# Kernel optimization log

Measured on AMD Instinct MI355X. Metric: run time of the kernel, lower is better.

## Reference

```python
import jax, jax.numpy as jnp
import numpy as np

C = 256
NUM_HEADS = 8
GROUPS = 32
EPS = 1e-5


def setup_inputs() -> dict:
    key = jax.random.key(0)
    ks = jax.random.split(key, 7)
    B, D, H, W = 1, 16, 16, 16
    x = jax.random.normal(ks[0], (B, C, D, H, W), dtype=jnp.float32)
    # GroupNorm affine params (torch default: weight=1, bias=0; randomize slightly)
    gn_gamma = 1.0 + 0.02 * jax.random.normal(ks[1], (C,), dtype=jnp.float32)
    gn_beta = 0.02 * jax.random.normal(ks[2], (C,), dtype=jnp.float32)
    # 1x1x1 Conv3d == pointwise linear over channels
    qkv_w = jax.random.normal(ks[3], (3 * C, C), dtype=jnp.float32) / np.sqrt(C)
    qkv_b = 0.01 * jax.random.normal(ks[4], (3 * C,), dtype=jnp.float32)
    proj_w = jax.random.normal(ks[5], (C, C), dtype=jnp.float32) / np.sqrt(C)
    proj_b = 0.01 * jax.random.normal(ks[6], (C,), dtype=jnp.float32)
    return {"x": x, "gn_gamma": gn_gamma, "gn_beta": gn_beta,
            "qkv_w": qkv_w, "qkv_b": qkv_b, "proj_w": proj_w, "proj_b": proj_b}


def _group_norm(x, gamma, beta):
    B, Cc, D, H, W = x.shape
    xg = x.reshape(B, GROUPS, -1)  # [B, G, (C/G)*D*H*W]
    mean = xg.mean(axis=2, keepdims=True)
    var = xg.var(axis=2, keepdims=True)
    xn = ((xg - mean) * jax.lax.rsqrt(var + EPS)).reshape(B, Cc, D, H, W)
    return xn * gamma[None, :, None, None, None] + beta[None, :, None, None, None]


def reference(x, gn_gamma, gn_beta, qkv_w, qkv_b, proj_w, proj_b):
    B, Cc, D, H, W = x.shape
    N = D * H * W
    heads = NUM_HEADS
    hd = Cc // heads
    scale = hd ** -0.5

    xn = _group_norm(x, gn_gamma, gn_beta)
    # 1x1x1 conv -> pointwise linear over channel dim
    h = jnp.einsum('bcn,oc->bon', xn.reshape(B, Cc, N), qkv_w) + qkv_b[None, :, None]
    # match torch: reshape(B,3,heads,hd,N).permute(1,0,2,4,3)
    qkv = h.reshape(B, 3, heads, hd, N).transpose(1, 0, 2, 4, 3)  # [3,B,heads,N,hd]
    q, k, v = qkv[0], qkv[1], qkv[2]
    attn = jax.nn.softmax(jnp.einsum('bhnd,bhmd->bhnm', q, k) * scale, axis=-1)
    out = jnp.einsum('bhnm,bhmd->bhnd', attn, v)  # [B,heads,N,hd]
    # match torch: transpose(1,2).reshape(B,C,D,H,W)
    out = out.transpose(0, 2, 1, 3).reshape(B, Cc, D, H, W)
    out = jnp.einsum('bcn,oc->bon', out.reshape(B, Cc, N), proj_w) + proj_b[None, :, None]
    return x + out.reshape(B, Cc, D, H, W)
```

## Files before the change

### kernel.cpp

```cpp
#include <hip/hip_runtime.h>
#include <hip/hip_bf16.h>
#include <cstddef>
#include <cstdint>

#define NTOK 4096
#define CCH  256
#define HEADS 8
#define HD    32
#define QSCALE 0.25503494f

typedef __attribute__((ext_vector_type(8)))  short short8;
typedef __attribute__((ext_vector_type(4)))  short short4v;
typedef __attribute__((ext_vector_type(16))) float f32x16;

__device__ __forceinline__ unsigned short f2bf(float x) {
    unsigned u = __builtin_bit_cast(unsigned, x);
    u = (u + 0x7fffu + ((u >> 16) & 1u)) >> 16;
    return (unsigned short)u;
}
__device__ __forceinline__ unsigned packbf2(float a, float b) {
    unsigned r;
    asm("v_cvt_pk_bf16_f32 %0, %1, %2" : "=v"(r) : "v"(a), "v"(b));
    return r;
}
__device__ __forceinline__ float exp2hw(float x) {
    float r;
    asm("v_exp_f32 %0, %1" : "=v"(r) : "v"(x));
    return r;
}

#define CROW(r, hi) (((r) & 3) + 8 * ((r) >> 2) + 4 * (hi))

__global__ __launch_bounds__(256) void gn_part_kernel(
    const float* __restrict__ X, float2* __restrict__ part)
{
    int c = blockIdx.x, tid = threadIdx.x;
    const float4* xr = (const float4*)(X + (size_t)c * NTOK);
    float s = 0.f, ss = 0.f;
    #pragma unroll
    for (int i = 0; i < 4; i++) {
        float4 v = xr[tid + i * 256];
        s  += (v.x + v.y) + (v.z + v.w);
        ss += (v.x*v.x + v.y*v.y) + (v.z*v.z + v.w*v.w);
    }
    #pragma unroll
    for (int off = 32; off >= 1; off >>= 1) {
        s  += __shfl_down(s, off, 64);
        ss += __shfl_down(ss, off, 64);
    }
    __shared__ float rs[4], rss[4];
    int wid = tid >> 6, lane = tid & 63;
    if (lane == 0) { rs[wid] = s; rss[wid] = ss; }
    __syncthreads();
    if (tid == 0) {
        part[c] = make_float2(rs[0] + rs[1] + rs[2] + rs[3],
                              rss[0] + rss[1] + rss[2] + rss[3]);
    }
}

__global__ __launch_bounds__(256) void prep_kernel(
    const float* __restrict__ X, const float2* __restrict__ part,
    const float* __restrict__ gamma, const float* __restrict__ beta,
    const float* __restrict__ qkvw, const float* __restrict__ projw,
    unsigned short* __restrict__ Xt, unsigned short* __restrict__ Wqb,
    unsigned short* __restrict__ Wpb)
{
    int bi = blockIdx.x, tid = threadIdx.x;
    if (bi >= 256) {
        const float* src; unsigned short* dst;
        if (bi < 268) { src = qkvw + (size_t)(bi - 256) * 16384; dst = Wqb + (size_t)(bi - 256) * 16384; }
        else          { src = projw + (size_t)(bi - 268) * 16384; dst = Wpb + (size_t)(bi - 268) * 16384; }
        #pragma unroll
        for (int i = 0; i < 16; i++) {
            float4 v = *(const float4*)(src + (size_t)tid * 4 + (size_t)i * 1024);
            short4v w;
            w[0] = (short)f2bf(v.x); w[1] = (short)f2bf(v.y);
            w[2] = (short)f2bf(v.z); w[3] = (short)f2bf(v.w);
            *(short4v*)(dst + (size_t)tid * 4 + (size_t)i * 1024) = w;
        }
        return;
    }
    __shared__ float plds[64 * 65];
    __shared__ float gmean[8], grstd[8];
    int ci = bi >> 6, ni = bi & 63;
    if (tid < 8) {
        int g = ci * 8 + tid;
        float s = 0.f, ss = 0.f;
        #pragma unroll
        for (int k = 0; k < 8; k++) {
            float2 p = part[g * 8 + k];
            s += p.x; ss += p.y;
        }
        float mean = s * (1.f / 32768.f);
        float var  = ss * (1.f / 32768.f) - mean * mean;
        gmean[tid] = mean;
        grstd[tid] = rsqrtf(var + 1e-5f);
    }
    __syncthreads();
    #pragma unroll
    for (int i = 0; i < 4; i++) {
        int cl = (tid >> 4) + i * 16;
        int c  = ci * 64 + cl;
        int gl = cl >> 3;
        float scv = gamma[c] * grstd[gl];
        float tcv = beta[c] - gmean[gl] * scv;
        float4 v = *(const float4*)(X + (size_t)c * NTOK + ni * 64 + (tid & 15) * 4);
        float* row = plds + cl * 65 + (tid & 15) * 4;
        row[0] = v.x * scv + tcv; row[1] = v.y * scv + tcv;
        row[2] = v.z * scv + tcv; row[3] = v.w * scv + tcv;
    }
    __syncthreads();
    int nw = tid >> 2, c4 = (tid & 3) * 16;
    unsigned short tmp[16];
    #pragma unroll
    for (int i = 0; i < 16; i++) tmp[i] = f2bf(plds[(c4 + i) * 65 + nw]);
    unsigned short* dst = Xt + (size_t)(ni * 64 + nw) * CCH + ci * 64 + c4;
    *(short8*)dst       = *(short8*)&tmp[0];
    *(short8*)(dst + 8) = *(short8*)&tmp[8];
}

__global__ __launch_bounds__(256) void qkv_mfma_kernel(
    const unsigned short* __restrict__ Wqb, const unsigned short* __restrict__ Xt,
    const float* __restrict__ qkvb,
    unsigned short* __restrict__ Qb, unsigned short* __restrict__ Kbf,
    unsigned short* __restrict__ Vtb)
{
    __shared__ __align__(16) char vlds[16384];
    const int tid = threadIdx.x;
    const int wid = tid >> 6, lane = tid & 63;
    const int l31 = lane & 31, hi = lane >> 5;
    const int bo = blockIdx.x >> 5, ng = blockIdx.x & 31;
    const int o0 = bo * 32;
    const int n0 = ng * 128 + wid * 32;

    const unsigned short* ap = Xt + (size_t)(n0 + l31) * CCH + hi * 8;
    const unsigned short* bp = Wqb + (size_t)(o0 + l31) * CCH + hi * 8;

    f32x16 acc;
    #pragma unroll
    for (int i = 0; i < 16; i++) acc[i] = 0.f;
    #pragma unroll 4
    for (int ks = 0; ks < 16; ks++) {
        short8 af = *(const short8*)(ap + ks * 16);
        short8 bf = *(const short8*)(bp + ks * 16);
        acc = __builtin_amdgcn_mfma_f32_32x32x16_bf16(af, bf, acc, 0, 0, 0);
    }

    const int t3 = bo >> 3;
    const int h  = (o0 >> 5) & 7;
    const float bias = qkvb[o0 + l31];

    if (t3 != 2) {
        unsigned short* dst = ((t3 == 0) ? Qb : Kbf) + (size_t)h * NTOK * HD + l31;
        const float scl = (t3 == 0) ? QSCALE : 1.0f;
        #pragma unroll
        for (int r = 0; r < 16; r++) {
            int n = n0 + CROW(r, hi);
            dst[(size_t)n * HD] = f2bf((acc[r] + bias) * scl);
        }
    } else {
        char* my = vlds + wid * 4096;
        #pragma unroll
        for (int r = 0; r < 16; r++) {
            int row = CROW(r, hi);
            *(float*)(my + row * 128 + ((l31 * 4) ^ ((row & 7) << 4))) = acc[r] + bias;
        }
        unsigned short tmp[16];
        #pragma unroll
        for (int i = 0; i < 16; i++) {
            int n = hi * 16 + i;
            tmp[i] = f2bf(*(const float*)(my + n * 128 + ((l31 * 4) ^ ((n & 7) << 4))));
        }
        unsigned short* vd = Vtb + ((size_t)h * HD + l31) * NTOK + n0 + hi * 16;
        *(short8*)vd       = *(short8*)&tmp[0];
        *(short8*)(vd + 8) = *(short8*)&tmp[8];
    }
}

__global__ __launch_bounds__(256) void attn_mfma_kernel(
    const unsigned short* __restrict__ Qb, const unsigned short* __restrict__ Kbf,
    const unsigned short* __restrict__ Vtb, unsigned short* __restrict__ att_t)
{
    __shared__ float stash[4][64][37];
    __shared__ float lsum[4][64];
    const int tid = threadIdx.x;
    const int wid = tid >> 6, lane = tid & 63;
    const int l31 = lane & 31, hi = lane >> 5;
    const int bid = blockIdx.x;
    const int h    = bid & 7;
    const int g    = bid >> 3;
    const int base = g & 15;
    const int j0   = (g >> 4) * 64;

    const unsigned short* kp = Kbf + ((size_t)h * NTOK + wid * 1024 + l31) * HD + hi * 8;
    const unsigned short* vp = Vtb + ((size_t)h * HD + l31) * NTOK + wid * 1024 + hi * 8;

    const unsigned short* qpA = Qb + ((size_t)h * NTOK + base + 16 * (size_t)(j0 + l31)) * HD + hi * 8;
    const unsigned short* qpB = qpA + (size_t)32 * 16 * HD;
    short8 qfA0 = *(const short8*)qpA;
    short8 qfA1 = *(const short8*)(qpA + 16);
    short8 qfB0 = *(const short8*)qpB;
    short8 qfB1 = *(const short8*)(qpB + 16);

    f32x16 oaccA, oaccB;
    #pragma unroll
    for (int i = 0; i < 16; i++) { oaccA[i] = 0.f; oaccB[i] = 0.f; }
    const f32x16 zero = oaccA;
    float lA = 0.f, lB = 0.f;

#define ATTN_BODY(KF0, KF1, VF0, VF1) do {                                     \
    f32x16 sA = __builtin_amdgcn_mfma_f32_32x32x16_bf16(KF0, qfA0, zero, 0, 0, 0); \
    sA = __builtin_amdgcn_mfma_f32_32x32x16_bf16(KF1, qfA1, sA, 0, 0, 0);      \
    f32x16 sB = __builtin_amdgcn_mfma_f32_32x32x16_bf16(KF0, qfB0, zero, 0, 0, 0); \
    sB = __builtin_amdgcn_mfma_f32_32x32x16_bf16(KF1, qfB1, sB, 0, 0, 0);      \
    float pA[16], pB[16];                                                      \
    _Pragma("unroll") for (int r = 0; r < 16; r++) pA[r] = exp2hw(sA[r]);      \
    _Pragma("unroll") for (int r = 0; r < 16; r++) pB[r] = exp2hw(sB[r]);      \
    lA += (((pA[0]+pA[1]) + (pA[2]+pA[3])) + ((pA[4]+pA[5]) + (pA[6]+pA[7])))  \
        + (((pA[8]+pA[9]) + (pA[10]+pA[11])) + ((pA[12]+pA[13]) + (pA[14]+pA[15]))); \
    lB += (((pB[0]+pB[1]) + (pB[2]+pB[3])) + ((pB[4]+pB[5]) + (pB[6]+pB[7])))  \
        + (((pB[8]+pB[9]) + (pB[10]+pB[11])) + ((pB[12]+pB[13]) + (pB[14]+pB[15]))); \
    _Pragma("unroll")                                                          \
    for (int m = 0; m < 2; m++) {                                              \
        const int b8 = m * 8;                                                  \
        unsigned A0 = packbf2(pA[b8 + 0], pA[b8 + 1]);                         \
        unsigned A1 = packbf2(pA[b8 + 2], pA[b8 + 3]);                         \
        unsigned B0 = packbf2(pA[b8 + 4], pA[b8 + 5]);                         \
        unsigned B1 = packbf2(pA[b8 + 6], pA[b8 + 7]);                         \
        asm volatile("v_permlane32_swap_b32 %0, %1" : "+v"(A0), "+v"(B0));     \
        asm volatile("v_permlane32_swap_b32 %0, %1" : "+v"(A1), "+v"(B1));     \
        union { unsigned u[4]; short8 v; } pa;                                 \
        pa.u[0] = A0; pa.u[1] = A1; pa.u[2] = B0; pa.u[3] = B1;                \
        oaccA = __builtin_amdgcn_mfma_f32_32x32x16_bf16(                       \
            pa.v, (m == 0) ? (VF0) : (VF1), oaccA, 0, 0, 0);                   \
    }                                                                          \
    _Pragma("unroll")                                                          \
    for (int m = 0; m < 2; m++) {                                              \
        const int b8 = m * 8;                                                  \
        unsigned A0 = packbf2(pB[b8 + 0], pB[b8 + 1]);                         \
        unsigned A1 = packbf2(pB[b8 + 2], pB[b8 + 3]);                         \
        unsigned B0 = packbf2(pB[b8 + 4], pB[b8 + 5]);                         \
        unsigned B1 = packbf2(pB[b8 + 6], pB[b8 + 7]);                         \
        asm volatile("v_permlane32_swap_b32 %0, %1" : "+v"(A0), "+v"(B0));     \
        asm volatile("v_permlane32_swap_b32 %0, %1" : "+v"(A1), "+v"(B1));     \
        union { unsigned u[4]; short8 v; } pa;                                 \
        pa.u[0] = A0; pa.u[1] = A1; pa.u[2] = B0; pa.u[3] = B1;                \
        oaccB = __builtin_amdgcn_mfma_f32_32x32x16_bf16(                       \
            pa.v, (m == 0) ? (VF0) : (VF1), oaccB, 0, 0, 0);                   \
    }                                                                          \
} while (0)

    short8 kf0a = *(const short8*)(kp);
    short8 kf1a = *(const short8*)(kp + 16);
    short8 vf0a = *(const short8*)(vp);
    short8 vf1a = *(const short8*)(vp + 16);

    #pragma unroll 1
    for (int t = 0; t < 32; t += 2) {
        const int t1 = t + 1;
        short8 kf0b = *(const short8*)(kp + t1 * 1024);
        short8 kf1b = *(const short8*)(kp + t1 * 1024 + 16);
        short8 vf0b = *(const short8*)(vp + t1 * 32);
        short8 vf1b = *(const short8*)(vp + t1 * 32 + 16);
        ATTN_BODY(kf0a, kf1a, vf0a, vf1a);
        const int t2 = (t + 2 < 32) ? (t + 2) : 31;
        kf0a = *(const short8*)(kp + t2 * 1024);
        kf1a = *(const short8*)(kp + t2 * 1024 + 16);
        vf0a = *(const short8*)(vp + t2 * 32);
        vf1a = *(const short8*)(vp + t2 * 32 + 16);
        ATTN_BODY(kf0b, kf1b, vf0b, vf1b);
    }
#undef ATTN_BODY

    lA += __shfl_xor(lA, 32, 64);
    lB += __shfl_xor(lB, 32, 64);
    #pragma unroll
    for (int r = 0; r < 16; r++) {
        int rowA = CROW(r, hi);
        stash[wid][rowA][l31] = oaccA[r];
        stash[wid][rowA + 32][l31] = oaccB[r];
    }
    if (lane < 32) { lsum[wid][l31] = lA; lsum[wid][32 + l31] = lB; }
    __syncthreads();

    const int d = tid >> 3, q8 = (tid & 7) * 8;
    unsigned short ob[8];
    #pragma unroll
    for (int i = 0; i < 8; i++) {
        int q = q8 + i;
        float lt = (lsum[0][q] + lsum[1][q]) + (lsum[2][q] + lsum[3][q]);
        float a = (stash[0][q][d] + stash[1][q][d]) + (stash[2][q][d] + stash[3][q][d]);
        ob[i] = f2bf(a / lt);
    }
    unsigned short* dst = att_t + (size_t)(base * 256 + h * 32 + d) * CCH + j0 + q8;
    *(short8*)dst = *(short8*)ob;
}

__global__ __launch_bounds__(256) void proj_mfma_kernel(
    const unsigned short* __restrict__ Wpb, const unsigned short* __restrict__ att_t,
    const float* __restrict__ X, const float* __restrict__ pb,
    float* __restrict__ out)
{
    const int tid = threadIdx.x;
    const int wid = tid >> 6, lane = tid & 63;
    const int l31 = lane & 31, hi = lane >> 5;
    const int ot = blockIdx.x >> 5, pg = blockIdx.x & 31;
    const int o0 = ot * 32;
    const int p0 = pg * 128 + wid * 32;

    const unsigned short* ap = Wpb + (size_t)(o0 + l31) * CCH + hi * 8;
    const unsigned short* bp = att_t + (size_t)(p0 + l31) * CCH + hi * 8;

    f32x16 acc;
    #pragma unroll
    for (int i = 0; i < 16; i++) acc[i] = 0.f;
    #pragma unroll 4
    for (int ks = 0; ks < 16; ks++) {
        short8 af = *(const short8*)(ap + ks * 16);
        short8 bf = *(const short8*)(bp + ks * 16);
        acc = __builtin_amdgcn_mfma_f32_32x32x16_bf16(af, bf, acc, 0, 0, 0);
    }
    #pragma unroll
    for (int r = 0; r < 16; r++) {
        int o = o0 + CROW(r, hi);
        size_t ofs = (size_t)o * NTOK + p0 + l31;
        out[ofs] = X[ofs] + pb[o] + acc[r];
    }
}

extern "C" void kernel_launch(void* const* d_in, const int* in_sizes, int n_in,
                              void* d_out, int out_size, void* d_ws, size_t ws_size,
                              hipStream_t stream)
{
    const float* x     = (const float*)d_in[0];
    const float* gamma = (const float*)d_in[1];
    const float* beta  = (const float*)d_in[2];
    const float* qkvw  = (const float*)d_in[3];
    const float* qkvb  = (const float*)d_in[4];
    const float* projw = (const float*)d_in[5];
    const float* projb = (const float*)d_in[6];
    float* out = (float*)d_out;

    char* ws = (char*)d_ws;
    const size_t MB = 1024 * 1024;
    float2* part = (float2*)ws;
    unsigned short* Xt    = (unsigned short*)(ws + 4096);
    unsigned short* Wqb   = (unsigned short*)(ws + 4096 + 2*MB);
    unsigned short* Wpb   = Wqb + 768 * 256;
    unsigned short* Qb    = Wpb + 256 * 256;
    unsigned short* Kbf   = Qb + HEADS * NTOK * HD;
    unsigned short* Vtb   = Kbf + HEADS * NTOK * HD;
    unsigned short* att_t = Vtb + HEADS * NTOK * HD;

    gn_part_kernel<<<256, 256, 0, stream>>>(x, part);
    prep_kernel<<<272, 256, 0, stream>>>(x, part, gamma, beta, qkvw, projw, Xt, Wqb, Wpb);
    qkv_mfma_kernel<<<768, 256, 0, stream>>>(Wqb, Xt, qkvb, Qb, Kbf, Vtb);
    attn_mfma_kernel<<<512, 256, 0, stream>>>(Qb, Kbf, Vtb, att_t);
    proj_mfma_kernel<<<256, 256, 0, stream>>>(Wpb, att_t, x, projb, out);
}
```

Before: 62.59 us.

## Split attention key range across eight waves per block instead of four

The attention kernel now launches 512 threads per block, so eight waves each process half as many key tiles, and the cross-wave reduction of partial outputs and row sums covers eight stashes. The register double-buffered prefetch of K/V fragments is replaced by loading both tiles at the top of each iteration. The aim is more wavefronts in flight to hide memory latency and a shorter serial loop per wave. In exchange the block uses twice the shared memory, does a larger LDS reduction, and loses the cross-iteration prefetch.

Measured after the change: 108.9 us. 74.0% more time.

```diff
diff --git a/kernel.cpp b/kernel.cpp
--- a/kernel.cpp
+++ b/kernel.cpp
@@ -177,12 +177,12 @@
     }
 }
 
-__global__ __launch_bounds__(256) void attn_mfma_kernel(
+__global__ __launch_bounds__(512, 4) void attn_mfma_kernel(
     const unsigned short* __restrict__ Qb, const unsigned short* __restrict__ Kbf,
     const unsigned short* __restrict__ Vtb, unsigned short* __restrict__ att_t)
 {
-    __shared__ float stash[4][64][37];
-    __shared__ float lsum[4][64];
+    __shared__ float stash[8][64][37];
+    __shared__ float lsum[8][64];
     const int tid = threadIdx.x;
     const int wid = tid >> 6, lane = tid & 63;
     const int l31 = lane & 31, hi = lane >> 5;
@@ -192,8 +192,8 @@
     const int base = g & 15;
     const int j0   = (g >> 4) * 64;
 
-    const unsigned short* kp = Kbf + ((size_t)h * NTOK + wid * 1024 + l31) * HD + hi * 8;
-    const unsigned short* vp = Vtb + ((size_t)h * HD + l31) * NTOK + wid * 1024 + hi * 8;
+    const unsigned short* kp = Kbf + ((size_t)h * NTOK + wid * 512 + l31) * HD + hi * 8;
+    const unsigned short* vp = Vtb + ((size_t)h * HD + l31) * NTOK + wid * 512 + hi * 8;
 
     const unsigned short* qpA = Qb + ((size_t)h * NTOK + base + 16 * (size_t)(j0 + l31)) * HD + hi * 8;
     const unsigned short* qpB = qpA + (size_t)32 * 16 * HD;
@@ -250,24 +250,17 @@
     }                                                                          \
 } while (0)
 
-    short8 kf0a = *(const short8*)(kp);
-    short8 kf1a = *(const short8*)(kp + 16);
-    short8 vf0a = *(const short8*)(vp);
-    short8 vf1a = *(const short8*)(vp + 16);
-
     #pragma unroll 1
-    for (int t = 0; t < 32; t += 2) {
-        const int t1 = t + 1;
-        short8 kf0b = *(const short8*)(kp + t1 * 1024);
-        short8 kf1b = *(const short8*)(kp + t1 * 1024 + 16);
-        short8 vf0b = *(const short8*)(vp + t1 * 32);
-        short8 vf1b = *(const short8*)(vp + t1 * 32 + 16);
+    for (int t = 0; t < 16; t += 2) {
+        short8 kf0a = *(const short8*)(kp + t * 1024);
+        short8 kf1a = *(const short8*)(kp + t * 1024 + 16);
+        short8 vf0a = *(const short8*)(vp + t * 32);
+        short8 vf1a = *(const short8*)(vp + t * 32 + 16);
+        short8 kf0b = *(const short8*)(kp + (t + 1) * 1024);
+        short8 kf1b = *(const short8*)(kp + (t + 1) * 1024 + 16);
+        short8 vf0b = *(const short8*)(vp + (t + 1) * 32);
+        short8 vf1b = *(const short8*)(vp + (t + 1) * 32 + 16);
         ATTN_BODY(kf0a, kf1a, vf0a, vf1a);
-        const int t2 = (t + 2 < 32) ? (t + 2) : 31;
-        kf0a = *(const short8*)(kp + t2 * 1024);
-        kf1a = *(const short8*)(kp + t2 * 1024 + 16);
-        vf0a = *(const short8*)(vp + t2 * 32);
-        vf1a = *(const short8*)(vp + t2 * 32 + 16);
         ATTN_BODY(kf0b, kf1b, vf0b, vf1b);
     }
 #undef ATTN_BODY
@@ -283,17 +276,19 @@
     if (lane < 32) { lsum[wid][l31] = lA; lsum[wid][32 + l31] = lB; }
     __syncthreads();
 
-    const int d = tid >> 3, q8 = (tid & 7) * 8;
-    unsigned short ob[8];
-    #pragma unroll
-    for (int i = 0; i < 8; i++) {
-        int q = q8 + i;
-        float lt = (lsum[0][q] + lsum[1][q]) + (lsum[2][q] + lsum[3][q]);
-        float a = (stash[0][q][d] + stash[1][q][d]) + (stash[2][q][d] + stash[3][q][d]);
+    const int d = tid >> 4, q4 = (tid & 15) * 4;
+    unsigned short ob[4];
+    #pragma unroll
+    for (int i = 0; i < 4; i++) {
+        int q = q4 + i;
+        float lt = ((lsum[0][q] + lsum[1][q]) + (lsum[2][q] + lsum[3][q]))
+                 + ((lsum[4][q] + lsum[5][q]) + (lsum[6][q] + lsum[7][q]));
+        float a = ((stash[0][q][d] + stash[1][q][d]) + (stash[2][q][d] + stash[3][q][d]))
+                + ((stash[4][q][d] + stash[5][q][d]) + (stash[6][q][d] + stash[7][q][d]));
         ob[i] = f2bf(a / lt);
     }
-    unsigned short* dst = att_t + (size_t)(base * 256 + h * 32 + d) * CCH + j0 + q8;
-    *(short8*)dst = *(short8*)ob;
+    unsigned short* dst = att_t + (size_t)(base * 256 + h * 32 + d) * CCH + j0 + q4;
+    *(short4v*)dst = *(short4v*)ob;
 }
 
 __global__ __launch_bounds__(256) void proj_mfma_kernel(
@@ -355,6 +350,6 @@
     gn_part_kernel<<<256, 256, 0, stream>>>(x, part);
     prep_kernel<<<272, 256, 0, stream>>>(x, part, gamma, beta, qkvw, projw, Xt, Wqb, Wpb);
     qkv_mfma_kernel<<<768, 256, 0, stream>>>(Wqb, Xt, qkvb, Qb, Kbf, Vtb);
-    attn_mfma_kernel<<<512, 256, 0, stream>>>(Qb, Kbf, Vtb, att_t);
+    attn_mfma_kernel<<<512, 512, 0, stream>>>(Qb, Kbf, Vtb, att_t);
     proj_mfma_kernel<<<256, 256, 0, stream>>>(Wpb, att_t, x, projb, out);
 }
```
